# Optimization experiments

Measured on AMD Instinct MI355X. Metric: run time of the kernel, lower is better.

Reference implementation:

```python
import jax, jax.numpy as jnp
import numpy as np

NEG_SLOPE = 0.2  # DGL GATConv default leaky_relu slope


def gat_conv(x_src, x_dst, src, dst, W, al, ar, b, n_dst):
    """DGL-style GATConv (shared fc for src/dst), returns [n_dst, H, D]."""
    H, D = al.shape
    fs = (x_src @ W).reshape(-1, H, D)            # [Ns, H, D]
    fd = (x_dst @ W).reshape(-1, H, D)            # [Nd, H, D]
    el = jnp.einsum('nhd,hd->nh', fs, al)          # [Ns, H]
    er = jnp.einsum('nhd,hd->nh', fd, ar)          # [Nd, H]
    e = jax.nn.leaky_relu(el[src] + er[dst], NEG_SLOPE)  # [E, H]
    m = jax.ops.segment_max(e, dst, num_segments=n_dst)
    m = jax.lax.stop_gradient(jnp.where(jnp.isfinite(m), m, 0.0))
    ex = jnp.exp(e - m[dst])
    s = jax.ops.segment_sum(ex, dst, num_segments=n_dst)
    alpha = ex / s[dst]                            # edge softmax per dst node
    out = jax.ops.segment_sum(alpha[:, :, None] * fs[src], dst, num_segments=n_dst)
    return out + b.reshape(1, H, D)


def setup_inputs() -> dict:
    key = jax.random.key(0)
    ks = jax.random.split(key, 16)
    Np, Na, E = 100000, 50000, 500000
    in_dim, h, H, D, out_dim = 128, 256, 4, 64, 192
    f = jax.random.normal
    return {
        'x_paper': f(ks[0], (Np, in_dim), jnp.float32),
        'x_author': f(ks[1], (Na, in_dim), jnp.float32),
        'W0': f(ks[2], (3, in_dim, h), jnp.float32) / np.float32(np.sqrt(in_dim)),
        'al0': f(ks[3], (3, H, D), jnp.float32) * 0.1,
        'ar0': f(ks[4], (3, H, D), jnp.float32) * 0.1,
        'b0': jnp.zeros((3, h), jnp.float32),
        'W1': f(ks[5], (3, h, h), jnp.float32) / np.float32(np.sqrt(h)),
        'al1': f(ks[6], (3, H, D), jnp.float32) * 0.1,
        'ar1': f(ks[7], (3, H, D), jnp.float32) * 0.1,
        'b1': jnp.zeros((3, h), jnp.float32),
        'lin_w': f(ks[8], (h, out_dim), jnp.float32) / np.float32(np.sqrt(h)),
        'lin_b': jnp.zeros((out_dim,), jnp.float32),
        'src_cites': jax.random.randint(ks[9], (E,), 0, Np, jnp.int32),
        'dst_cites': jax.random.randint(ks[10], (E,), 0, Np, jnp.int32),
        'src_writes': jax.random.randint(ks[11], (E,), 0, Na, jnp.int32),
        'dst_writes': jax.random.randint(ks[12], (E,), 0, Np, jnp.int32),
        'src_written': jax.random.randint(ks[13], (E,), 0, Np, jnp.int32),
        'dst_written': jax.random.randint(ks[14], (E,), 0, Na, jnp.int32),
    }


def reference(x_paper, x_author, W0, al0, ar0, b0, W1, al1, ar1, b1,
              lin_w, lin_b, src_cites, dst_cites, src_writes, dst_writes,
              src_written, dst_written):
    Np, Na = x_paper.shape[0], x_author.shape[0]

    def layer(hp, ha, W, al, ar, b):
        # HeteroGraphConv: sum over relations sharing the same dst ntype.
        p = gat_conv(hp, hp, src_cites, dst_cites, W[0], al[0], ar[0], b[0], Np) \
          + gat_conv(ha, hp, src_writes, dst_writes, W[1], al[1], ar[1], b[1], Np)
        a = gat_conv(hp, ha, src_written, dst_written, W[2], al[2], ar[2], b[2], Na)
        # view(N, heads*out)
        return p.reshape(Np, -1), a.reshape(Na, -1)

    hp, ha = layer(x_paper, x_author, W0, al0, ar0, b0)
    hp, ha = jax.nn.relu(hp), jax.nn.relu(ha)  # dropout = identity (eval mode)
    hp, ha = layer(hp, ha, W1, al1, ar1, b1)
    return hp @ lin_w + lin_b  # self.lin(h['paper'])
```

## Files before the change

### kernel.cpp

```cpp
#include <hip/hip_runtime.h>

typedef unsigned short u16;
typedef unsigned int u32;
typedef __attribute__((ext_vector_type(8))) short bf16x8;
typedef __attribute__((ext_vector_type(4))) float f32x4;

static __device__ __forceinline__ float bf2f(u16 u) {
  union { unsigned int i; float f; } v; v.i = ((unsigned int)u) << 16; return v.f;
}
static __device__ __forceinline__ u16 f2bf(float f) {
  union { float f; unsigned int i; } v; v.f = f;
  unsigned int i = v.i;
  return (u16)((i + 0x7FFFu + ((i >> 16) & 1u)) >> 16);
}

static __device__ __forceinline__ void gl16(const u16* g, u16* l) {
  __builtin_amdgcn_global_load_lds(
      (const __attribute__((address_space(1))) unsigned int*)g,
      (__attribute__((address_space(3))) unsigned int*)l, 16, 0, 0);
}

__global__ __launch_bounds__(256) void cvt2(const float* __restrict__ a, const float* __restrict__ b,
                                            u16* __restrict__ da, u16* __restrict__ db,
                                            int n4a, int n4b)
{
  int i = blockIdx.x * 256 + threadIdx.x;
  const float* s; u16* d; int j;
  if (i < n4a) { s = a; d = da; j = i; }
  else { j = i - n4a; if (j >= n4b) return; s = b; d = db; }
  float4 v = ((const float4*)s)[j];
  ushort4 r;
  r.x = f2bf(v.x); r.y = f2bf(v.y); r.z = f2bf(v.z); r.w = f2bf(v.w);
  ((ushort4*)d)[j] = r;
}

__global__ __launch_bounds__(256) void transpose3(const float* __restrict__ src,
                                                  u16* __restrict__ dst, int R, int K, int N)
{
  int idx = blockIdx.x * 256 + threadIdx.x;
  if (idx >= R * K * N) return;
  int r = idx / (K * N), rem = idx - r * K * N;
  int k = rem / N, n = rem - k * N;
  dst[(size_t)r * N * K + (size_t)n * K + k] = f2bf(src[idx]);
}

__global__ __launch_bounds__(256) void build_wr2(
    const float* __restrict__ Wa, const float* __restrict__ Wb,
    const float* __restrict__ ara, const float* __restrict__ arb,
    float* __restrict__ wra, float* __restrict__ wrb, int K)
{
  int idx = blockIdx.x * 256 + threadIdx.x;
  if (idx >= 2 * K * 4) return;
  int sel = idx / (K * 4), rem = idx - sel * K * 4;
  int k = rem >> 2, h = rem & 3;
  const float* W = sel ? Wb : Wa;
  const float* ar = sel ? arb : ara;
  float s = 0.f;
  for (int d = 0; d < 64; ++d)
    s += W[(size_t)k * 256 + h * 64 + d] * ar[h * 64 + d];
  (sel ? wrb : wra)[rem] = s;
}

template<int K, int NTW>
__global__ __launch_bounds__(256, 3) void gemm_rb(
    const u16* __restrict__ X, const u16* __restrict__ Wt,
    u16* __restrict__ out16, float* __restrict__ out32,
    const float* __restrict__ bias,
    const float* __restrict__ al4, const float* __restrict__ ar4,
    float* __restrict__ el, float* __restrict__ er, int M)
{
  constexpr int NS = K / 64;
  const int N = NTW * 16 * 4;
  __shared__ __align__(16) u16 As[2][64 * 64];
  const int t = threadIdx.x;
  const int wave = t >> 6, lane = t & 63;
  const int quad = lane >> 4, l16 = lane & 15;
  const int mbase = blockIdx.x * 64;
  const int nbase = wave * (NTW * 16);

  int r0 = t >> 3, r1 = 32 + (t >> 3);
  int c0 = (t & 7) ^ (r0 & 7);
  int c1 = (t & 7) ^ (r1 & 7);
  int rr0 = mbase + r0; if (rr0 >= M) rr0 = M - 1;
  int rr1 = mbase + r1; if (rr1 >= M) rr1 = M - 1;
  const u16* g0 = X + (size_t)rr0 * K + c0 * 8;
  const u16* g1 = X + (size_t)rr1 * K + c1 * 8;

  const u16* wp = Wt + (size_t)(nbase + l16) * K + quad * 8;

  f32x4 acc[4][NTW];
#pragma unroll
  for (int mt = 0; mt < 4; ++mt)
#pragma unroll
    for (int nt = 0; nt < NTW; ++nt) acc[mt][nt] = (f32x4){0.f, 0.f, 0.f, 0.f};

  bf16x8 bb[2][NTW];

  auto stage_a = [&](int s, int b) {
    gl16(g0 + s * 64, &As[b][t * 8]);
    gl16(g1 + s * 64, &As[b][2048 + t * 8]);
  };
  auto load_b = [&](int s) {
#pragma unroll
    for (int kk = 0; kk < 2; ++kk)
#pragma unroll
      for (int nt = 0; nt < NTW; ++nt)
        bb[kk][nt] = *(const bf16x8*)(wp + (size_t)nt * 16 * K + s * 64 + kk * 32);
  };

  stage_a(0, 0);
  __builtin_amdgcn_sched_barrier(0);
  load_b(0);
  __builtin_amdgcn_sched_barrier(0);
  if (NS > 1) stage_a(1, 1);
  __builtin_amdgcn_sched_barrier(0);

  const int sw = (l16 & 7) << 3;
#pragma unroll
  for (int ks = 0; ks < NS; ++ks) {
    if (ks + 1 < NS) asm volatile("s_waitcnt vmcnt(2)" ::: "memory");
    else             asm volatile("s_waitcnt vmcnt(0)" ::: "memory");
    __builtin_amdgcn_s_barrier();
    __builtin_amdgcn_sched_barrier(0);
    const u16* Ab = As[ks & 1];
#pragma unroll
    for (int kk = 0; kk < 2; ++kk) {
      bf16x8 a[4];
#pragma unroll
      for (int mt = 0; mt < 4; ++mt)
        a[mt] = *(const bf16x8*)(Ab + (mt * 16 + l16) * 64 + ((kk * 32 + quad * 8) ^ sw));
#pragma unroll
      for (int mt = 0; mt < 4; ++mt)
#pragma unroll
        for (int nt = 0; nt < NTW; ++nt)
          acc[mt][nt] = __builtin_amdgcn_mfma_f32_16x16x32_bf16(a[mt], bb[kk][nt], acc[mt][nt], 0, 0, 0);
    }
    if (ks + 1 < NS) load_b(ks + 1);
    __builtin_amdgcn_sched_barrier(0);
    __builtin_amdgcn_s_barrier();
    __builtin_amdgcn_sched_barrier(0);
    if (ks + 2 < NS) {
      stage_a(ks + 2, ks & 1);
      __builtin_amdgcn_sched_barrier(0);
    }
  }

#pragma unroll
  for (int mt = 0; mt < 4; ++mt)
#pragma unroll
    for (int nt = 0; nt < NTW; ++nt) {
      int col = nbase + nt * 16 + l16;
      float bv = bias ? bias[col] : 0.f;
#pragma unroll
      for (int r = 0; r < 4; ++r) {
        int row = mbase + mt * 16 + quad * 4 + r;
        if (row < M) {
          float v = acc[mt][nt][r] + bv;
          if (out32) out32[(size_t)row * N + col] = v;
          else       out16[(size_t)row * N + col] = f2bf(v);
        }
      }
    }
  if (al4 != nullptr) {
    float alv[NTW], arv[NTW];
#pragma unroll
    for (int nt = 0; nt < NTW; ++nt) {
      alv[nt] = al4[wave * 64 + nt * 16 + l16];
      arv[nt] = ar4 ? ar4[wave * 64 + nt * 16 + l16] : 0.f;
    }
#pragma unroll
    for (int mt = 0; mt < 4; ++mt) {
#pragma unroll
      for (int r = 0; r < 4; ++r) {
        float p = 0.f, q = 0.f;
#pragma unroll
        for (int nt = 0; nt < NTW; ++nt) {
          p += acc[mt][nt][r] * alv[nt];
          q += acc[mt][nt][r] * arv[nt];
        }
#pragma unroll
        for (int off = 1; off < 16; off <<= 1) {
          p += __shfl_xor(p, off);
          q += __shfl_xor(q, off);
        }
        int row = mbase + mt * 16 + quad * 4 + r;
        if (l16 == 0 && row < M) {
          el[row * 4 + wave] = p;
          if (ar4) er[row * 4 + wave] = q;
        }
      }
    }
  }
}

__global__ __launch_bounds__(256) void er_wr2(
    const u16* __restrict__ Xp, const u16* __restrict__ Xa,
    const float* __restrict__ wrp, const float* __restrict__ wra,
    float* __restrict__ erp, float* __restrict__ era, int Np, int Na, int K)
{
  int nblkP = (Np + 3) / 4;
  int bid = blockIdx.x;
  const u16* X; const float* wr; float* er; int nid, Nn;
  if (bid < nblkP) { X = Xp; wr = wrp; er = erp; Nn = Np; nid = bid * 4 + (threadIdx.x >> 6); }
  else { X = Xa; wr = wra; er = era; Nn = Na; nid = (bid - nblkP) * 4 + (threadIdx.x >> 6); }
  if (nid >= Nn) return;
  int lane = threadIdx.x & 63;
  float a0 = 0.f, a1 = 0.f, a2 = 0.f, a3 = 0.f;
  for (int k = lane; k < K; k += 64) {
    float xv = bf2f(X[(size_t)nid * K + k]);
    const float* w = wr + k * 4;
    a0 += xv * w[0]; a1 += xv * w[1]; a2 += xv * w[2]; a3 += xv * w[3];
  }
  for (int off = 1; off < 64; off <<= 1) {
    a0 += __shfl_xor(a0, off); a1 += __shfl_xor(a1, off);
    a2 += __shfl_xor(a2, off); a3 += __shfl_xor(a3, off);
  }
  if (lane == 0) {
    er[nid * 4 + 0] = a0; er[nid * 4 + 1] = a1;
    er[nid * 4 + 2] = a2; er[nid * 4 + 3] = a3;
  }
}


__global__ __launch_bounds__(256) void zero3(int* p, int n) {
  int i = blockIdx.x * 256 + threadIdx.x;
  if (i < n) p[i] = 0;
}

__global__ __launch_bounds__(256) void p1hist(
    const int* __restrict__ dC, const int* __restrict__ dW, const int* __restrict__ dR,
    int E, int NBC, int* __restrict__ bcnt)
{
  int nbE = (E + 4095) >> 12;
  int bi = blockIdx.x, rel = bi / nbE, ch = bi - rel * nbE;
  const int* d = rel == 0 ? dC : (rel == 1 ? dW : dR);
  int rbase = rel * NBC;
  int e0 = ch << 12, e1 = min(E, e0 + 4096);
  __shared__ int cnt[128];
  int t = threadIdx.x;
  if (t < 128) cnt[t] = 0;
  __syncthreads();
  for (int e = e0 + t; e < e1; e += 256) atomicAdd(&cnt[d[e] >> 10], 1);
  __syncthreads();
  if (t < 128) { int n = cnt[t]; if (n) atomicAdd(&bcnt[rbase + t], n); }
}

__global__ __launch_bounds__(1024) void bscan(
    const int* __restrict__ bcnt, int* __restrict__ bbase, int* __restrict__ gcur, int nb)
{
  __shared__ int sm[1024];
  int t = threadIdx.x;
  int v = (t < nb) ? bcnt[t] : 0;
  sm[t] = v; __syncthreads();
  for (int off = 1; off < 1024; off <<= 1) {
    int add = (t >= off) ? sm[t - off] : 0;
    __syncthreads();
    sm[t] += add;
    __syncthreads();
  }
  if (t < nb) { int e = sm[t] - v; bbase[t] = e; gcur[t] = e; }
}

__global__ __launch_bounds__(256) void p1scat(
    const int* __restrict__ sC, const int* __restrict__ dC,
    const int* __restrict__ sW, const int* __restrict__ dW,
    const int* __restrict__ sR, const int* __restrict__ dR,
    int E, int NBC, int* __restrict__ gcur, u32* __restrict__ stage3)
{
  int nbE = (E + 4095) >> 12;
  int bi = blockIdx.x, rel = bi / nbE, ch = bi - rel * nbE;
  const int *s, *d;
  if (rel == 0) { s = sC; d = dC; }
  else if (rel == 1) { s = sW; d = dW; }
  else { s = sR; d = dR; }
  int rbase = rel * NBC;
  int e0 = ch << 12, e1 = min(E, e0 + 4096);
  __shared__ int cnt[128], cur[128], gpos[128];
  int t = threadIdx.x;
  if (t < 128) { cnt[t] = 0; cur[t] = 0; }
  __syncthreads();
  for (int e = e0 + t; e < e1; e += 256) atomicAdd(&cnt[d[e] >> 10], 1);
  __syncthreads();
  if (t < 128) { int n = cnt[t]; gpos[t] = n ? atomicAdd(&gcur[rbase + t], n) : 0; }
  __syncthreads();
  for (int e = e0 + t; e < e1; e += 256) {
    int dd = d[e], b = dd >> 10;
    int slot = atomicAdd(&cur[b], 1);
    stage3[gpos[b] + slot] = (u32)(s[e] & 0x3FFFF) | ((u32)(dd & 1023) << 18);
  }
}

__global__ __launch_bounds__(256) void p2fine(
    const u32* __restrict__ stage3, const int* __restrict__ bcnt, const int* __restrict__ bbase,
    int* __restrict__ rpC, int* __restrict__ rpW, int* __restrict__ rpR,
    int* __restrict__ srcsC, int* __restrict__ srcsW, int* __restrict__ srcsR,
    int E, int Np, int Na, int NBC)
{
  int bid = blockIdx.x, t = threadIdx.x;
  int rel, b, Nrel; int* rp; int* srcs;
  if (bid < NBC)          { rel = 0; b = bid;            Nrel = Np; rp = rpC; srcs = srcsC; }
  else if (bid < 2 * NBC) { rel = 1; b = bid - NBC;      Nrel = Np; rp = rpW; srcs = srcsW; }
  else                    { rel = 2; b = bid - 2 * NBC;  Nrel = Na; rp = rpR; srcs = srcsR; }
  int base = bbase[bid], cnt = bcnt[bid];
  int csrbase = base - rel * E;
  int dstbase = b << 10;
  int ndst = Nrel - dstbase; if (ndst > 1024) ndst = 1024;
  __shared__ int h[1024], cur[1024], tmp[256];
  for (int i = t; i < 1024; i += 256) h[i] = 0;
  __syncthreads();
  for (int i = t; i < cnt; i += 256) atomicAdd(&h[stage3[base + i] >> 18], 1);
  __syncthreads();
  int s4 = h[4 * t] + h[4 * t + 1] + h[4 * t + 2] + h[4 * t + 3];
  tmp[t] = s4; __syncthreads();
  for (int off = 1; off < 256; off <<= 1) {
    int add = (t >= off) ? tmp[t - off] : 0;
    __syncthreads();
    tmp[t] += add;
    __syncthreads();
  }
  int run = tmp[t] - s4;
#pragma unroll
  for (int j = 0; j < 4; ++j) { int hv = h[4 * t + j]; cur[4 * t + j] = run; run += hv; }
  __syncthreads();
  for (int d = t; d < ndst; d += 256) rp[dstbase + d] = csrbase + cur[d];
  if (bid == 0 && t == 0) { rpC[Np] = E; rpW[Np] = E; rpR[Na] = E; }
  __syncthreads();
  for (int i = t; i < cnt; i += 256) {
    u32 w = stage3[base + i];
    int lp = atomicAdd(&cur[w >> 18], 1);
    srcs[csrbase + lp] = (int)(w & 0x3FFFF);
  }
}

static __device__ __forceinline__ void pk2(float2& a, unsigned int u, float w) {
  union { unsigned int i; float f; } lo, hi;
  lo.i = u << 16; hi.i = u & 0xffff0000u;
  a.x += w * lo.f;
  a.y += w * hi.f;
}
static __device__ __forceinline__ void edge1(
    int sid, int sl, int hh, const float* __restrict__ el, float ern,
    const u16* __restrict__ fs, float2* acc2, float& sw)
{
  float v = el[(size_t)sid * 4 + hh] + ern;
  uint4 r = *(const uint4*)(fs + (size_t)sid * 256 + sl * 8);
  v = v > 0.f ? v : 0.2f * v;
  float w = __expf(v);
  sw += w;
  pk2(acc2[0], r.x, w); pk2(acc2[1], r.y, w);
  pk2(acc2[2], r.z, w); pk2(acc2[3], r.w, w);
}
static __device__ __forceinline__ void edge4(
    int sid0, int sid1, int sid2, int sid3, int sl, int hh,
    const float* __restrict__ el, float ern, const u16* __restrict__ fs,
    float2* acc2, float& sw)
{
  float v0 = el[(size_t)sid0 * 4 + hh] + ern;
  float v1 = el[(size_t)sid1 * 4 + hh] + ern;
  float v2 = el[(size_t)sid2 * 4 + hh] + ern;
  float v3 = el[(size_t)sid3 * 4 + hh] + ern;
  uint4 r0 = *(const uint4*)(fs + (size_t)sid0 * 256 + sl * 8);
  uint4 r1 = *(const uint4*)(fs + (size_t)sid1 * 256 + sl * 8);
  uint4 r2 = *(const uint4*)(fs + (size_t)sid2 * 256 + sl * 8);
  uint4 r3 = *(const uint4*)(fs + (size_t)sid3 * 256 + sl * 8);
  v0 = v0 > 0.f ? v0 : 0.2f * v0;
  v1 = v1 > 0.f ? v1 : 0.2f * v1;
  v2 = v2 > 0.f ? v2 : 0.2f * v2;
  v3 = v3 > 0.f ? v3 : 0.2f * v3;
  float w0 = __expf(v0), w1 = __expf(v1), w2 = __expf(v2), w3 = __expf(v3);
  sw += (w0 + w1) + (w2 + w3);
  pk2(acc2[0], r0.x, w0); pk2(acc2[1], r0.y, w0);
  pk2(acc2[2], r0.z, w0); pk2(acc2[3], r0.w, w0);
  pk2(acc2[0], r1.x, w1); pk2(acc2[1], r1.y, w1);
  pk2(acc2[2], r1.z, w1); pk2(acc2[3], r1.w, w1);
  pk2(acc2[0], r2.x, w2); pk2(acc2[1], r2.y, w2);
  pk2(acc2[2], r2.z, w2); pk2(acc2[3], r2.w, w2);
  pk2(acc2[0], r3.x, w3); pk2(acc2[1], r3.y, w3);
  pk2(acc2[2], r3.z, w3); pk2(acc2[3], r3.w, w3);
}

__global__ __launch_bounds__(256) void agg_paper(
    const int* __restrict__ rp0, const int* __restrict__ srcs0,
    const float* __restrict__ el0, const float* __restrict__ er0,
    const u16* __restrict__ fs0,
    const int* __restrict__ rp1, const int* __restrict__ srcs1,
    const float* __restrict__ el1, const float* __restrict__ er1,
    const u16* __restrict__ fs1,
    const float* __restrict__ bias0, const float* __restrict__ bias1,
    u16* __restrict__ out, int Nd, int relu)
{
  int nid = blockIdx.x * 4 + (threadIdx.x >> 6);
  if (nid >= Nd) return;
  int lane = threadIdx.x & 63;
  int half = lane >> 5, sl = lane & 31, hh = sl >> 3;
  const int* rp     = half ? rp1 : rp0;
  const int* srcs   = half ? srcs1 : srcs0;
  const float* el   = half ? el1 : el0;
  const float* er   = half ? er1 : er0;
  const u16* fs     = half ? fs1 : fs0;
  float ern = er[(size_t)nid * 4 + hh];
  int s0 = rp[nid], s1 = rp[nid + 1];
  float2 acc2[4] = {{0.f,0.f},{0.f,0.f},{0.f,0.f},{0.f,0.f}};
  float sw = 0.f;
  int i = s0;
  for (; i + 3 < s1; i += 4)
    edge4(srcs[i], srcs[i + 1], srcs[i + 2], srcs[i + 3], sl, hh, el, ern, fs, acc2, sw);
  for (; i < s1; ++i)
    edge1(srcs[i], sl, hh, el, ern, fs, acc2, sw);
  float inv = sw > 0.f ? 1.f / sw : 0.f;
  float o[8];
#pragma unroll
  for (int k = 0; k < 4; ++k) {
    o[2 * k]     = acc2[k].x * inv;
    o[2 * k + 1] = acc2[k].y * inv;
  }
#pragma unroll
  for (int j = 0; j < 8; ++j) o[j] += __shfl_xor(o[j], 32);
  if (half == 0) {
    const float* bp0 = bias0 + sl * 8;
    const float* bp1 = bias1 + sl * 8;
    bf16x8 r;
#pragma unroll
    for (int j = 0; j < 8; ++j) {
      float v = o[j] + bp0[j] + bp1[j];
      if (relu) v = fmaxf(v, 0.f);
      r[j] = (short)f2bf(v);
    }
    *(bf16x8*)(out + (size_t)nid * 256 + sl * 8) = r;
  }
}

__global__ __launch_bounds__(256) void agg_author(
    const int* __restrict__ rp0, const int* __restrict__ srcs0,
    const float* __restrict__ el0, const float* __restrict__ er0,
    const u16* __restrict__ fs0,
    const float* __restrict__ bias0, u16* __restrict__ out, int Nd, int relu)
{
  int nid = blockIdx.x * 4 + (threadIdx.x >> 6);
  if (nid >= Nd) return;
  int lane = threadIdx.x & 63;
  int half = lane >> 5, sl = lane & 31, hh = sl >> 3;
  float ern = er0[(size_t)nid * 4 + hh];
  int s0 = rp0[nid], s1 = rp0[nid + 1];
  float2 acc2[4] = {{0.f,0.f},{0.f,0.f},{0.f,0.f},{0.f,0.f}};
  float sw = 0.f;
  int i = s0 + half;
  for (; i + 6 < s1; i += 8)
    edge4(srcs0[i], srcs0[i + 2], srcs0[i + 4], srcs0[i + 6], sl, hh, el0, ern, fs0, acc2, sw);
  for (; i < s1; i += 2)
    edge1(srcs0[i], sl, hh, el0, ern, fs0, acc2, sw);
  sw += __shfl_xor(sw, 32);
  float inv = sw > 0.f ? 1.f / sw : 0.f;
  float o[8];
#pragma unroll
  for (int k = 0; k < 4; ++k) {
    o[2 * k]     = (acc2[k].x + __shfl_xor(acc2[k].x, 32)) * inv;
    o[2 * k + 1] = (acc2[k].y + __shfl_xor(acc2[k].y, 32)) * inv;
  }
  if (half == 0) {
    const float* bp0 = bias0 + sl * 8;
    bf16x8 r;
#pragma unroll
    for (int j = 0; j < 8; ++j) {
      float v = o[j] + bp0[j];
      if (relu) v = fmaxf(v, 0.f);
      r[j] = (short)f2bf(v);
    }
    *(bf16x8*)(out + (size_t)nid * 256 + sl * 8) = r;
  }
}

static inline int cdiv(int a, int b) { return (a + b - 1) / b; }

extern "C" void kernel_launch(void* const* d_in, const int* in_sizes, int n_in,
                              void* d_out, int out_size, void* d_ws, size_t ws_size,
                              hipStream_t stream)
{
  const float* xp   = (const float*)d_in[0];
  const float* xa   = (const float*)d_in[1];
  const float* W0   = (const float*)d_in[2];
  const float* al0  = (const float*)d_in[3];
  const float* ar0  = (const float*)d_in[4];
  const float* b0   = (const float*)d_in[5];
  const float* W1   = (const float*)d_in[6];
  const float* al1  = (const float*)d_in[7];
  const float* ar1  = (const float*)d_in[8];
  const float* b1   = (const float*)d_in[9];
  const float* linw = (const float*)d_in[10];
  const float* linb = (const float*)d_in[11];
  const int* srcC = (const int*)d_in[12];
  const int* dstC = (const int*)d_in[13];
  const int* srcW = (const int*)d_in[14];
  const int* dstW = (const int*)d_in[15];
  const int* srcR = (const int*)d_in[16];
  const int* dstR = (const int*)d_in[17];
  float* out = (float*)d_out;

  const int Np = in_sizes[0] / 128;
  const int Na = in_sizes[1] / 128;
  const int E  = in_sizes[12];

  char* base = (char*)d_ws;
  size_t off = 0;
  auto alloc = [&](size_t bytes) -> void* {
    void* r = base + off;
    off += (bytes + 255) & ~(size_t)255;
    return r;
  };
  u16* Wt0  = (u16*)alloc((size_t)3 * 256 * 128 * 2);
  u16* Wt1  = (u16*)alloc((size_t)3 * 256 * 256 * 2);
  u16* Wtl  = (u16*)alloc((size_t)192 * 256 * 2);
  float* wr01 = (float*)alloc(128 * 4 * 4);
  float* wr02 = (float*)alloc(128 * 4 * 4);
  float* wr11 = (float*)alloc(256 * 4 * 4);
  float* wr12 = (float*)alloc(256 * 4 * 4);
  u16* xpb  = (u16*)alloc((size_t)Np * 128 * 2);
  u16* xab  = (u16*)alloc((size_t)Na * 128 * 2);
  u16* fs0p = (u16*)alloc((size_t)Np * 256 * 2);
  u16* fs1a = (u16*)alloc((size_t)Na * 256 * 2);
  u16* fs2p = (u16*)alloc((size_t)Np * 256 * 2);
  u16* h1p  = (u16*)alloc((size_t)Np * 256 * 2);
  u16* h1a  = (u16*)alloc((size_t)Na * 256 * 2);
  float* el0 = (float*)alloc((size_t)Np * 4 * 4);
  float* er0 = (float*)alloc((size_t)Np * 4 * 4);
  float* el1 = (float*)alloc((size_t)Na * 4 * 4);
  float* er1 = (float*)alloc((size_t)Np * 4 * 4);
  float* el2 = (float*)alloc((size_t)Np * 4 * 4);
  float* er2 = (float*)alloc((size_t)Na * 4 * 4);
  int* rpC  = (int*)alloc((size_t)(Np + 1) * 4);
  int* rpW  = (int*)alloc((size_t)(Np + 1) * 4);
  int* rpR  = (int*)alloc((size_t)(Na + 1) * 4);
  int* srcsC = (int*)alloc((size_t)E * 4);
  int* srcsW = (int*)alloc((size_t)E * 4);
  int* srcsR = (int*)alloc((size_t)E * 4);
  int* bcnt  = (int*)alloc(1024 * 4);
  int* bbase = (int*)alloc(1024 * 4);
  int* gcur  = (int*)alloc(1024 * 4);
  u32* stage3 = (u32*)fs0p;

  cvt2<<<cdiv(Np * 32 + Na * 32, 256), 256, 0, stream>>>(xp, xa, xpb, xab, Np * 32, Na * 32);
  transpose3<<<cdiv(3 * 128 * 256, 256), 256, 0, stream>>>(W0, Wt0, 3, 128, 256);
  transpose3<<<cdiv(3 * 256 * 256, 256), 256, 0, stream>>>(W1, Wt1, 3, 256, 256);
  transpose3<<<cdiv(256 * 192, 256), 256, 0, stream>>>(linw, Wtl, 1, 256, 192);
  build_wr2<<<cdiv(2 * 128 * 4, 256), 256, 0, stream>>>(W0 + 32768, W0 + 65536,
                                                        ar0 + 256, ar0 + 512, wr01, wr02, 128);
  build_wr2<<<cdiv(2 * 256 * 4, 256), 256, 0, stream>>>(W1 + 65536, W1 + 131072,
                                                        ar1 + 256, ar1 + 512, wr11, wr12, 256);

  const int NBC = cdiv(Np, 1024);
  const int NBA = cdiv(Na, 1024);
  const int NBtot = 2 * NBC + NBA;
  const int nbE = cdiv(E, 4096);
  zero3<<<cdiv(NBtot, 256), 256, 0, stream>>>(bcnt, NBtot);
  p1hist<<<3 * nbE, 256, 0, stream>>>(dstC, dstW, dstR, E, NBC, bcnt);
  bscan<<<1, 1024, 0, stream>>>(bcnt, bbase, gcur, NBtot);
  p1scat<<<3 * nbE, 256, 0, stream>>>(srcC, dstC, srcW, dstW, srcR, dstR,
                                      E, NBC, gcur, stage3);
  p2fine<<<NBtot, 256, 0, stream>>>(stage3, bcnt, bbase, rpC, rpW, rpR,
                                    srcsC, srcsW, srcsR, E, Np, Na, NBC);

  auto layer = [&](const u16* inP, const u16* inA, const u16* WtL, int K,
                   const float* alL, const float* arL,
                   const float* wr1, const float* wr2, const float* bL,
                   u16* outP, u16* outA, int relu) {
    size_t wsz = (size_t)256 * K;
    if (K == 128) {
      gemm_rb<128, 4><<<dim3(cdiv(Np, 64)), 256, 0, stream>>>(
          inP, WtL, fs0p, nullptr, nullptr, alL, arL, el0, er0, Np);
      gemm_rb<128, 4><<<dim3(cdiv(Na, 64)), 256, 0, stream>>>(
          inA, WtL + wsz, fs1a, nullptr, nullptr, alL + 256, nullptr, el1, nullptr, Na);
      gemm_rb<128, 4><<<dim3(cdiv(Np, 64)), 256, 0, stream>>>(
          inP, WtL + 2 * wsz, fs2p, nullptr, nullptr, alL + 512, nullptr, el2, nullptr, Np);
    } else {
      gemm_rb<256, 4><<<dim3(cdiv(Np, 64)), 256, 0, stream>>>(
          inP, WtL, fs0p, nullptr, nullptr, alL, arL, el0, er0, Np);
      gemm_rb<256, 4><<<dim3(cdiv(Na, 64)), 256, 0, stream>>>(
          inA, WtL + wsz, fs1a, nullptr, nullptr, alL + 256, nullptr, el1, nullptr, Na);
      gemm_rb<256, 4><<<dim3(cdiv(Np, 64)), 256, 0, stream>>>(
          inP, WtL + 2 * wsz, fs2p, nullptr, nullptr, alL + 512, nullptr, el2, nullptr, Np);
    }
    er_wr2<<<cdiv(Np, 4) + cdiv(Na, 4), 256, 0, stream>>>(inP, inA, wr1, wr2, er1, er2, Np, Na, K);
    agg_paper<<<cdiv(Np, 4), 256, 0, stream>>>(rpC, srcsC, el0, er0, fs0p,
                                               rpW, srcsW, el1, er1, fs1a,
                                               bL, bL + 256, outP, Np, relu);
    agg_author<<<cdiv(Na, 4), 256, 0, stream>>>(rpR, srcsR, el2, er2, fs2p,
                                                bL + 512, outA, Na, relu);
  };

  layer(xpb, xab, Wt0, 128, al0, ar0, wr01, wr02, b0, h1p, h1a, 1);
  layer(h1p, h1a, Wt1, 256, al1, ar1, wr11, wr12, b1, h1p, h1a, 0);

  gemm_rb<256, 3><<<dim3(cdiv(Np, 64)), 256, 0, stream>>>(
      h1p, Wtl, nullptr, out, linb, nullptr, nullptr, nullptr, nullptr, Np);
}
```

Baseline: 916.4 us.

## Prefetch all A k-stages into LDS upfront and double-buffer B registers in GEMM

The GEMM's A tile now gets one LDS buffer per k-stage (K/64 of them). All stages are issued up front instead of being recycled through a double buffer, which removes the second barrier each iteration. B fragments are double-buffered in registers two stages ahead, and the per-stage vmcnt waits are adjusted to match. This deepens the memory pipeline to hide global latency, at the cost of more LDS (32KB for K=256) and more registers, which may reduce occupancy below the 3 blocks per SM requested.

```diff
diff --git a/kernel.cpp b/kernel.cpp
--- a/kernel.cpp
+++ b/kernel.cpp
@@ -18,6 +18,16 @@
   __builtin_amdgcn_global_load_lds(
       (const __attribute__((address_space(1))) unsigned int*)g,
       (__attribute__((address_space(3))) unsigned int*)l, 16, 0, 0);
+}
+
+template<int N> static __device__ __forceinline__ void vwait() {
+  if constexpr (N == 0)       asm volatile("s_waitcnt vmcnt(0)" ::: "memory");
+  else if constexpr (N == 6)  asm volatile("s_waitcnt vmcnt(6)" ::: "memory");
+  else if constexpr (N == 8)  asm volatile("s_waitcnt vmcnt(8)" ::: "memory");
+  else if constexpr (N == 10) asm volatile("s_waitcnt vmcnt(10)" ::: "memory");
+  else if constexpr (N == 12) asm volatile("s_waitcnt vmcnt(12)" ::: "memory");
+  else if constexpr (N == 14) asm volatile("s_waitcnt vmcnt(14)" ::: "memory");
+  else                        asm volatile("s_waitcnt vmcnt(0)" ::: "memory");
 }
 
 __global__ __launch_bounds__(256) void cvt2(const float* __restrict__ a, const float* __restrict__ b,
@@ -70,8 +80,9 @@
     float* __restrict__ el, float* __restrict__ er, int M)
 {
   constexpr int NS = K / 64;
+  constexpr int LB = 2 * NTW;
   const int N = NTW * 16 * 4;
-  __shared__ __align__(16) u16 As[2][64 * 64];
+  __shared__ __align__(16) u16 As[NS][64 * 64];
   const int t = threadIdx.x;
   const int wave = t >> 6, lane = t & 63;
   const int quad = lane >> 4, l16 = lane & 15;
@@ -94,35 +105,44 @@
 #pragma unroll
     for (int nt = 0; nt < NTW; ++nt) acc[mt][nt] = (f32x4){0.f, 0.f, 0.f, 0.f};
 
-  bf16x8 bb[2][NTW];
-
-  auto stage_a = [&](int s, int b) {
-    gl16(g0 + s * 64, &As[b][t * 8]);
-    gl16(g1 + s * 64, &As[b][2048 + t * 8]);
+  bf16x8 bb[2][2][NTW];
+
+  auto stage_a = [&](int s) {
+    gl16(g0 + s * 64, &As[s][t * 8]);
+    gl16(g1 + s * 64, &As[s][2048 + t * 8]);
   };
-  auto load_b = [&](int s) {
+  auto load_b = [&](int s, int buf) {
 #pragma unroll
     for (int kk = 0; kk < 2; ++kk)
 #pragma unroll
       for (int nt = 0; nt < NTW; ++nt)
-        bb[kk][nt] = *(const bf16x8*)(wp + (size_t)nt * 16 * K + s * 64 + kk * 32);
+        bb[buf][kk][nt] = *(const bf16x8*)(wp + (size_t)nt * 16 * K + s * 64 + kk * 32);
   };
 
-  stage_a(0, 0);
+  stage_a(0);
   __builtin_amdgcn_sched_barrier(0);
-  load_b(0);
+  load_b(0, 0);
   __builtin_amdgcn_sched_barrier(0);
-  if (NS > 1) stage_a(1, 1);
+  stage_a(1);
   __builtin_amdgcn_sched_barrier(0);
+  load_b(1, 1);
+  __builtin_amdgcn_sched_barrier(0);
+  if constexpr (NS == 4) {
+    stage_a(2);
+    stage_a(3);
+    __builtin_amdgcn_sched_barrier(0);
+  }
 
   const int sw = (l16 & 7) << 3;
 #pragma unroll
   for (int ks = 0; ks < NS; ++ks) {
-    if (ks + 1 < NS) asm volatile("s_waitcnt vmcnt(2)" ::: "memory");
-    else             asm volatile("s_waitcnt vmcnt(0)" ::: "memory");
+    if (ks == 0)      vwait<(NS == 4 ? 6 + LB : 2 + LB)>();
+    else if (ks == 1) { if constexpr (NS == 4) vwait<4 + LB>(); else vwait<0>(); }
+    else if (ks == 2) vwait<LB>();
+    else              vwait<0>();
     __builtin_amdgcn_s_barrier();
     __builtin_amdgcn_sched_barrier(0);
-    const u16* Ab = As[ks & 1];
+    const u16* Ab = As[ks];
 #pragma unroll
     for (int kk = 0; kk < 2; ++kk) {
       bf16x8 a[4];
@@ -133,16 +153,10 @@
       for (int mt = 0; mt < 4; ++mt)
 #pragma unroll
         for (int nt = 0; nt < NTW; ++nt)
-          acc[mt][nt] = __builtin_amdgcn_mfma_f32_16x16x32_bf16(a[mt], bb[kk][nt], acc[mt][nt], 0, 0, 0);
+          acc[mt][nt] = __builtin_amdgcn_mfma_f32_16x16x32_bf16(a[mt], bb[ks & 1][kk][nt], acc[mt][nt], 0, 0, 0);
     }
-    if (ks + 1 < NS) load_b(ks + 1);
+    if (ks + 2 < NS) load_b(ks + 2, ks & 1);
     __builtin_amdgcn_sched_barrier(0);
-    __builtin_amdgcn_s_barrier();
-    __builtin_amdgcn_sched_barrier(0);
-    if (ks + 2 < NS) {
-      stage_a(ks + 2, ks & 1);
-      __builtin_amdgcn_sched_barrier(0);
-    }
   }
 
 #pragma unroll
```

Result: slower. 950.2 us (+3.7%).
